# Kernel optimization log

Hardware: AMD Instinct MI355X
Metric: run time of the kernel (lower is better)

Reference implementation:

```python
import jax, jax.numpy as jnp
import numpy as np

N, D, H, O, E = 50000, 128, 256, 128, 800000


def setup_inputs() -> dict:
    key = jax.random.key(0)
    ks = jax.random.split(key, 8)
    x = jax.random.normal(ks[0], (N, D), dtype=jnp.float32)
    edge_index = jax.random.randint(ks[1], (2, E), 0, N, dtype=jnp.int64)
    s = lambda k, shp: jax.random.normal(k, shp, dtype=jnp.float32) / np.sqrt(shp[0])
    return {
        "x": x,
        "edge_index": edge_index,
        "W1_l": s(ks[2], (D, H)),
        "W1_r": s(ks[3], (D, H)),
        "b1": jnp.zeros((H,), jnp.float32),
        "W2_l": s(ks[4], (H, O)),
        "W2_r": s(ks[5], (H, O)),
        "b2": jnp.zeros((O,), jnp.float32),
    }


def _sage_conv(x, src, dst, W_l, W_r, b, n_nodes):
    # mean aggregation of source messages into destination nodes
    agg = jax.ops.segment_sum(x[src], dst, num_segments=n_nodes)  # [N, F]
    cnt = jax.ops.segment_sum(jnp.ones(src.shape[0], x.dtype), dst,
                              num_segments=n_nodes)               # [N]
    agg = agg / jnp.maximum(cnt, 1.0)[:, None]
    # lin_l(agg) + lin_r(x); lin_l carries the bias (PyG SAGEConv default)
    return agg @ W_l + b + x @ W_r


def reference(x, edge_index, W1_l, W1_r, b1, W2_l, W2_r, b2):
    src, dst = edge_index[0], edge_index[1]
    h = jax.nn.relu(_sage_conv(x, src, dst, W1_l, W1_r, b1, N))
    out = _sage_conv(h, src, dst, W2_l, W2_r, b2, N)
    return out
```

## Files before the change

kernel.cpp:

```cpp
#include <hip/hip_runtime.h>


#define CAP 64
#define NB 98
#define BSH 9
#define BCAP 9216
#define CHUNK 2048

typedef __attribute__((ext_vector_type(8))) short short8;
typedef __attribute__((ext_vector_type(8))) unsigned short ushort8;
typedef __attribute__((ext_vector_type(4))) float f32x4;

__device__ __forceinline__ unsigned short f2bf(float f) {
  unsigned u = __builtin_bit_cast(unsigned, f);
  u += 0x7fff + ((u >> 16) & 1);
  return (unsigned short)(u >> 16);
}
__device__ __forceinline__ float bf2f(unsigned v) {
  return __builtin_bit_cast(float, v << 16);
}

__global__ __launch_bounds__(256) void bucket_kernel(
    const int* __restrict__ src, const int* __restrict__ dst,
    int* __restrict__ bcursor, unsigned* __restrict__ buckets, int E) {
  __shared__ unsigned pack[CHUNK];
  __shared__ unsigned char binarr[CHUNK];
  __shared__ unsigned sorted[CHUNK];
  __shared__ unsigned char sbin[CHUNK];
  __shared__ int hist[NB];
  __shared__ int scn[NB + 1];
  __shared__ int gbase[NB];
  const int t = threadIdx.x;
  const int e0 = blockIdx.x * CHUNK;
  const int n = min(CHUNK, E - e0);

  for (int i = t; i < NB; i += 256) hist[i] = 0;
  __syncthreads();
  for (int i = t; i < n; i += 256) {
    int s = src[e0 + i];
    int d = dst[e0 + i];
    int b = d >> BSH;
    pack[i] = ((unsigned)(d & 511) << 16) | (unsigned)s;
    binarr[i] = (unsigned char)b;
    atomicAdd(&hist[b], 1);
  }
  __syncthreads();
  if (t == 0) {
    int a = 0;
    for (int b = 0; b < NB; ++b) { scn[b] = a; a += hist[b]; }
    scn[NB] = a;
  }
  __syncthreads();
  if (t < NB) { gbase[t] = atomicAdd(&bcursor[t], hist[t]); hist[t] = 0; }
  __syncthreads();
  for (int i = t; i < n; i += 256) {
    int b = binarr[i];
    int pos = scn[b] + atomicAdd(&hist[b], 1);
    sorted[pos] = pack[i];
    sbin[pos] = (unsigned char)b;
  }
  __syncthreads();
  for (int i = t; i < n; i += 256) {
    int b = sbin[i];
    int off = gbase[b] + (i - scn[b]);
    if (off < BCAP) buckets[(size_t)b * BCAP + off] = sorted[i];
  }
}

__global__ __launch_bounds__(256) void csr_kernel(
    const int* __restrict__ bcursor, const unsigned* __restrict__ buckets,
    unsigned short* __restrict__ elist, int* __restrict__ deg, int N) {
  __shared__ unsigned short csr[128 * CAP];
  __shared__ int cur[128];
  const int t = threadIdx.x;
  const int b = blockIdx.x >> 2;
  const int q = blockIdx.x & 3;
  if (t < 128) cur[t] = 0;
  __syncthreads();
  const int cnt = min(bcursor[b], BCAP);
  const unsigned* bp = buckets + (size_t)b * BCAP;
  for (int i = t; i < cnt; i += 256) {
    unsigned p = bp[i];
    int lo = p >> 16;
    if ((lo >> 7) == q) {
      int r = lo & 127;
      int pos = atomicAdd(&cur[r], 1);
      if (pos < CAP) csr[r * CAP + pos] = (unsigned short)(p & 0xffffu);
    }
  }
  __syncthreads();
  const int node0 = (b << BSH) + (q << 7);
  const int nn = min(128, N - node0);
  if (nn <= 0) return;
  if (t < nn) deg[node0 + t] = min(cur[t], CAP);
  int4* dst4 = reinterpret_cast<int4*>(elist + (size_t)node0 * CAP);
  const int4* src4 = reinterpret_cast<const int4*>(csr);
  for (int i = t; i < nn * 8; i += 256) dst4[i] = src4[i];
}

__global__ __launch_bounds__(256) void convert_x_kernel(const float* __restrict__ x,
                                                        unsigned short* __restrict__ xb,
                                                        int* __restrict__ bcursor,
                                                        int n8) {
  int i = blockIdx.x * 256 + threadIdx.x;
  if (blockIdx.x == 0 && threadIdx.x < 128) bcursor[threadIdx.x] = 0;
  if (i >= n8) return;
  const float4* p = reinterpret_cast<const float4*>(x) + (size_t)i * 2;
  float4 a = p[0], b = p[1];
  union { unsigned short u[8]; int4 v; } r;
  r.u[0]=f2bf(a.x); r.u[1]=f2bf(a.y); r.u[2]=f2bf(a.z); r.u[3]=f2bf(a.w);
  r.u[4]=f2bf(b.x); r.u[5]=f2bf(b.y); r.u[6]=f2bf(b.z); r.u[7]=f2bf(b.w);
  reinterpret_cast<int4*>(xb)[i] = r.v;
}

__global__ __launch_bounds__(256) void convert_w_kernel(
    const float* __restrict__ W1l, const float* __restrict__ W1r,
    const float* __restrict__ W2l, const float* __restrict__ W2r,
    unsigned short* __restrict__ Wt1, unsigned short* __restrict__ Wt2) {
  int idx = blockIdx.x * 256 + threadIdx.x;
  int ch = idx >> 8, k = idx & 255;
  float v1 = (k < 128) ? W1l[k * 256 + ch] : W1r[(k - 128) * 256 + ch];
  Wt1[idx] = f2bf(v1);
  float v2 = (ch < 128) ? W2l[k * 128 + ch] : W2r[k * 128 + (ch - 128)];
  Wt2[idx] = f2bf(v2);
}

template<int MODE>
__global__ __launch_bounds__(256) void aggregate_kernel(
    const unsigned short* __restrict__ feat, const int* __restrict__ deg_,
    const unsigned short* __restrict__ elist, const unsigned short* __restrict__ hr,
    const float* __restrict__ bias, void* __restrict__ outp, int N) {
  const int node = (blockIdx.x * blockDim.x + threadIdx.x) >> 6;
  const int lane = threadIdx.x & 63;
  if (node >= N) return;
  const int deg = deg_[node];
  const unsigned short* el = elist + (size_t)node * CAP;
  const unsigned* f = reinterpret_cast<const unsigned*>(feat);
  float s0x=0.f,s0y=0.f,s1x=0.f,s1y=0.f,s2x=0.f,s2y=0.f,s3x=0.f,s3y=0.f;
  int j = 0;
  for (; j + 7 < deg; j += 8) {
    ushort8 e8 = *reinterpret_cast<const ushort8*>(el + j);
    unsigned v0 = f[(size_t)e8[0] * 64 + lane];
    unsigned v1 = f[(size_t)e8[1] * 64 + lane];
    unsigned v2 = f[(size_t)e8[2] * 64 + lane];
    unsigned v3 = f[(size_t)e8[3] * 64 + lane];
    unsigned v4 = f[(size_t)e8[4] * 64 + lane];
    unsigned v5 = f[(size_t)e8[5] * 64 + lane];
    unsigned v6 = f[(size_t)e8[6] * 64 + lane];
    unsigned v7 = f[(size_t)e8[7] * 64 + lane];
    s0x += bf2f(v0 & 0xffffu); s0y += bf2f(v0 >> 16);
    s1x += bf2f(v1 & 0xffffu); s1y += bf2f(v1 >> 16);
    s2x += bf2f(v2 & 0xffffu); s2y += bf2f(v2 >> 16);
    s3x += bf2f(v3 & 0xffffu); s3y += bf2f(v3 >> 16);
    s0x += bf2f(v4 & 0xffffu); s0y += bf2f(v4 >> 16);
    s1x += bf2f(v5 & 0xffffu); s1y += bf2f(v5 >> 16);
    s2x += bf2f(v6 & 0xffffu); s2y += bf2f(v6 >> 16);
    s3x += bf2f(v7 & 0xffffu); s3y += bf2f(v7 >> 16);
  }
  for (; j < deg; ++j) {
    unsigned v0 = f[(size_t)el[j] * 64 + lane];
    s0x += bf2f(v0 & 0xffffu); s0y += bf2f(v0 >> 16);
  }
  float inv = 1.0f / (float)max(deg, 1);
  float rx = (s0x + s1x + s2x + s3x) * inv;
  float ry = (s0y + s1y + s2y + s3y) * inv;
  if constexpr (MODE == 0) {
    unsigned r = (unsigned)f2bf(rx) | ((unsigned)f2bf(ry) << 16);
    reinterpret_cast<unsigned*>(outp)[(size_t)node * 64 + lane] = r;
  } else {
    unsigned res = reinterpret_cast<const unsigned*>(hr)[(size_t)node * 64 + lane];
    float2 bb = reinterpret_cast<const float2*>(bias)[lane];
    float2 o;
    o.x = rx + bf2f(res & 0xffffu) + bb.x;
    o.y = ry + bf2f(res >> 16) + bb.y;
    reinterpret_cast<float2*>(outp)[(size_t)node * 64 + lane] = o;
  }
}

__global__ __launch_bounds__(256, 2) void fused_gemm_kernel(
    const unsigned short* __restrict__ aggb, const unsigned short* __restrict__ xb,
    const unsigned short* __restrict__ Wt1, const unsigned short* __restrict__ Wt2,
    const float* __restrict__ b1,
    unsigned short* __restrict__ hw, unsigned short* __restrict__ hr, int N) {
  __shared__ int4 As4[512];
  __shared__ int4 Bs4[2048];
  __shared__ int4 hL4[2048];
  char* As = reinterpret_cast<char*>(As4);
  char* Bs = reinterpret_cast<char*>(Bs4);
  char* hL = reinterpret_cast<char*>(hL4);
  const int t = threadIdx.x;
  const int lane = t & 63;
  const int hi = lane >> 4;
  const int lo = lane & 15;
  const int wv = t >> 6;
  const int n0 = blockIdx.x * 64;
  const int cw = wv * 64;

  f32x4 acc[4][4];
  #pragma unroll
  for (int m = 0; m < 4; ++m)
    #pragma unroll
    for (int n = 0; n < 4; ++n)
      acc[m][n] = (f32x4){0.f, 0.f, 0.f, 0.f};

  for (int k0 = 0; k0 < 256; k0 += 64) {
    const unsigned short* Asrc = (k0 < 128) ? aggb : xb;
    const int kk0 = k0 & 127;
    #pragma unroll
    for (int i = 0; i < 2; ++i) {
      int chunk = i * 256 + t;
      int r = chunk >> 3, c16 = chunk & 7;
      int row = n0 + r; if (row >= N) row = N - 1;
      int4 v = *reinterpret_cast<const int4*>(Asrc + (size_t)row * 128 + kk0 + c16 * 8);
      *reinterpret_cast<int4*>(As + r * 128 + ((c16 * 16) ^ ((r & 7) << 4))) = v;
    }
    #pragma unroll
    for (int i = 0; i < 8; ++i) {
      int chunk = i * 256 + t;
      int cc = chunk >> 3, c16 = chunk & 7;
      int4 v = *reinterpret_cast<const int4*>(Wt1 + (size_t)cc * 256 + k0 + c16 * 8);
      *reinterpret_cast<int4*>(Bs + cc * 128 + ((c16 * 16) ^ ((cc & 7) << 4))) = v;
    }
    __syncthreads();
    #pragma unroll
    for (int kk = 0; kk < 64; kk += 32) {
      const int kb = (kk + hi * 8) * 2;
      short8 af[4], bfr[4];
      #pragma unroll
      for (int m = 0; m < 4; ++m) {
        int r = m * 16 + lo;
        af[m] = *reinterpret_cast<const short8*>(As + r * 128 + (kb ^ ((r & 7) << 4)));
      }
      #pragma unroll
      for (int n = 0; n < 4; ++n) {
        int c = cw + n * 16 + lo;
        bfr[n] = *reinterpret_cast<const short8*>(Bs + c * 128 + (kb ^ ((c & 7) << 4)));
      }
      #pragma unroll
      for (int m = 0; m < 4; ++m)
        #pragma unroll
        for (int n = 0; n < 4; ++n)
          acc[m][n] = __builtin_amdgcn_mfma_f32_16x16x32_bf16(af[m], bfr[n], acc[m][n], 0, 0, 0);
    }
    __syncthreads();
  }

  #pragma unroll
  for (int n = 0; n < 4; ++n) {
    const int col = cw + n * 16 + lo;
    const float bv = b1[col];
    const int seg = col >> 6;
    const int wb = (col & 63) * 2;
    #pragma unroll
    for (int m = 0; m < 4; ++m) {
      f32x4 v = acc[m][n];
      #pragma unroll
      for (int j = 0; j < 4; ++j) {
        int row = m * 16 + hi * 4 + j;
        float f = fmaxf(v[j] + bv, 0.0f);
        *reinterpret_cast<unsigned short*>(
            hL + row * 512 + seg * 128 + (wb ^ ((row & 7) << 4))) = f2bf(f);
      }
    }
  }
  __syncthreads();

  f32x4 acc2[4][4];
  #pragma unroll
  for (int m = 0; m < 4; ++m)
    #pragma unroll
    for (int n = 0; n < 4; ++n)
      acc2[m][n] = (f32x4){0.f, 0.f, 0.f, 0.f};

  for (int k0 = 0; k0 < 256; k0 += 64) {
    #pragma unroll
    for (int i = 0; i < 8; ++i) {
      int chunk = i * 256 + t;
      int cc = chunk >> 3, c16 = chunk & 7;
      int4 v = *reinterpret_cast<const int4*>(Wt2 + (size_t)cc * 256 + k0 + c16 * 8);
      *reinterpret_cast<int4*>(Bs + cc * 128 + ((c16 * 16) ^ ((cc & 7) << 4))) = v;
    }
    __syncthreads();
    #pragma unroll
    for (int kk = 0; kk < 64; kk += 32) {
      const int kb = (kk + hi * 8) * 2;
      short8 af[4], bfr[4];
      #pragma unroll
      for (int m = 0; m < 4; ++m) {
        int r = m * 16 + lo;
        af[m] = *reinterpret_cast<const short8*>(hL + r * 512 + k0 * 2 + (kb ^ ((r & 7) << 4)));
      }
      #pragma unroll
      for (int n = 0; n < 4; ++n) {
        int c = cw + n * 16 + lo;
        bfr[n] = *reinterpret_cast<const short8*>(Bs + c * 128 + (kb ^ ((c & 7) << 4)));
      }
      #pragma unroll
      for (int m = 0; m < 4; ++m)
        #pragma unroll
        for (int n = 0; n < 4; ++n)
          acc2[m][n] = __builtin_amdgcn_mfma_f32_16x16x32_bf16(af[m], bfr[n], acc2[m][n], 0, 0, 0);
    }
    __syncthreads();
  }

  unsigned short* dstp = (cw < 128) ? hw : hr;
  const int cbase = cw & 127;
  #pragma unroll
  for (int n = 0; n < 4; ++n) {
    const int col = cbase + n * 16 + lo;
    #pragma unroll
    for (int m = 0; m < 4; ++m) {
      f32x4 v = acc2[m][n];
      #pragma unroll
      for (int j = 0; j < 4; ++j) {
        int row = n0 + m * 16 + hi * 4 + j;
        if (row < N) dstp[(size_t)row * 128 + col] = f2bf(v[j]);
      }
    }
  }
}

extern "C" void kernel_launch(void* const* d_in, const int* in_sizes, int n_in,
                              void* d_out, int out_size, void* d_ws, size_t ws_size,
                              hipStream_t stream) {
  const float* x   = (const float*)d_in[0];
  const int*   ei  = (const int*)d_in[1];
  const float* W1l = (const float*)d_in[2];
  const float* W1r = (const float*)d_in[3];
  const float* b1  = (const float*)d_in[4];
  const float* W2l = (const float*)d_in[5];
  const float* W2r = (const float*)d_in[6];
  const float* b2  = (const float*)d_in[7];
  float* out = (float*)d_out;

  const int N = in_sizes[0] / 128;
  const int E = in_sizes[1] / 2;
  const int* src = ei;
  const int* dst = ei + E;

  int* iws = (int*)d_ws;
  int* bcursor = iws;
  unsigned* buckets = (unsigned*)(iws + 128);
  int* deg = (int*)(buckets + (size_t)NB * BCAP);
  unsigned short* elist = (unsigned short*)(deg + ((N + 64) & ~63));
  unsigned short* xb   = elist + (size_t)N * CAP;
  unsigned short* aggb = xb + (size_t)N * 128;
  unsigned short* hw   = aggb + (size_t)N * 128;
  unsigned short* hr   = hw + (size_t)N * 128;
  unsigned short* Wt1  = hr + (size_t)N * 128;
  unsigned short* Wt2  = Wt1 + 65536;

  convert_x_kernel<<<(N * 128 / 8 + 255) / 256, 256, 0, stream>>>(x, xb, bcursor, N * 128 / 8);
  convert_w_kernel<<<256, 256, 0, stream>>>(W1l, W1r, W2l, W2r, Wt1, Wt2);

  bucket_kernel<<<(E + CHUNK - 1) / CHUNK, 256, 0, stream>>>(src, dst, bcursor, buckets, E);
  csr_kernel<<<NB * 4, 256, 0, stream>>>(bcursor, buckets, elist, deg, N);

  const int aggBlocks = (N * 64 + 255) / 256;
  const int MB = (N + 63) / 64;

  aggregate_kernel<0><<<aggBlocks, 256, 0, stream>>>(xb, deg, elist, nullptr, nullptr, (void*)aggb, N);
  fused_gemm_kernel<<<MB, 256, 0, stream>>>(aggb, xb, Wt1, Wt2, b1, hw, hr, N);
  aggregate_kernel<1><<<aggBlocks, 256, 0, stream>>>(hw, deg, elist, hr, b2, (void*)out, N);
}
```

Baseline: 146.6 us.

## Fuse first-layer aggregation into GEMM kernel and merge conversion kernels

The first mean-aggregation is moved into the fused GEMM kernel: each block gathers neighbor features for its 64 rows directly into a combined LDS tile holding [agg | x], which is later reused for the hidden activations. This removes the aggb intermediate write and read and one kernel launch. The x and weight conversion kernels are also merged into one prep kernel. In exchange, the gather now runs inside a GEMM kernel limited by launch bounds to 2 blocks per CU, with only 4 waves handling 16 rows each, so latency hiding for the random gathers may be worse.

```diff
diff --git a/kernel.cpp b/kernel.cpp
--- a/kernel.cpp
+++ b/kernel.cpp
@@ -18,6 +18,33 @@
 }
 __device__ __forceinline__ float bf2f(unsigned v) {
   return __builtin_bit_cast(float, v << 16);
+}
+
+__global__ __launch_bounds__(256) void prep_kernel(
+    const float* __restrict__ x, unsigned short* __restrict__ xb,
+    const float* __restrict__ W1l, const float* __restrict__ W1r,
+    const float* __restrict__ W2l, const float* __restrict__ W2r,
+    unsigned short* __restrict__ Wt1, unsigned short* __restrict__ Wt2,
+    int* __restrict__ bcursor, int n8) {
+  const int b = blockIdx.x;
+  const int t = threadIdx.x;
+  if (b == 0 && t < 128) bcursor[t] = 0;
+  if (b < 256) {
+    int idx = b * 256 + t;
+    int ch = idx >> 8, k = idx & 255;
+    Wt1[idx] = f2bf((k < 128) ? W1l[k * 256 + ch] : W1r[(k - 128) * 256 + ch]);
+    Wt2[idx] = f2bf((ch < 128) ? W2l[k * 128 + ch] : W2r[k * 128 + (ch - 128)]);
+  } else {
+    int i = (b - 256) * 256 + t;
+    if (i < n8) {
+      const float4* p = reinterpret_cast<const float4*>(x) + (size_t)i * 2;
+      float4 a = p[0], bb = p[1];
+      union { unsigned short u[8]; int4 v; } r;
+      r.u[0]=f2bf(a.x); r.u[1]=f2bf(a.y); r.u[2]=f2bf(a.z); r.u[3]=f2bf(a.w);
+      r.u[4]=f2bf(bb.x); r.u[5]=f2bf(bb.y); r.u[6]=f2bf(bb.z); r.u[7]=f2bf(bb.w);
+      reinterpret_cast<int4*>(xb)[i] = r.v;
+    }
+  }
 }
 
 __global__ __launch_bounds__(256) void bucket_kernel(
@@ -98,38 +125,10 @@
   for (int i = t; i < nn * 8; i += 256) dst4[i] = src4[i];
 }
 
-__global__ __launch_bounds__(256) void convert_x_kernel(const float* __restrict__ x,
-                                                        unsigned short* __restrict__ xb,
-                                                        int* __restrict__ bcursor,
-                                                        int n8) {
-  int i = blockIdx.x * 256 + threadIdx.x;
-  if (blockIdx.x == 0 && threadIdx.x < 128) bcursor[threadIdx.x] = 0;
-  if (i >= n8) return;
-  const float4* p = reinterpret_cast<const float4*>(x) + (size_t)i * 2;
-  float4 a = p[0], b = p[1];
-  union { unsigned short u[8]; int4 v; } r;
-  r.u[0]=f2bf(a.x); r.u[1]=f2bf(a.y); r.u[2]=f2bf(a.z); r.u[3]=f2bf(a.w);
-  r.u[4]=f2bf(b.x); r.u[5]=f2bf(b.y); r.u[6]=f2bf(b.z); r.u[7]=f2bf(b.w);
-  reinterpret_cast<int4*>(xb)[i] = r.v;
-}
-
-__global__ __launch_bounds__(256) void convert_w_kernel(
-    const float* __restrict__ W1l, const float* __restrict__ W1r,
-    const float* __restrict__ W2l, const float* __restrict__ W2r,
-    unsigned short* __restrict__ Wt1, unsigned short* __restrict__ Wt2) {
-  int idx = blockIdx.x * 256 + threadIdx.x;
-  int ch = idx >> 8, k = idx & 255;
-  float v1 = (k < 128) ? W1l[k * 256 + ch] : W1r[(k - 128) * 256 + ch];
-  Wt1[idx] = f2bf(v1);
-  float v2 = (ch < 128) ? W2l[k * 128 + ch] : W2r[k * 128 + (ch - 128)];
-  Wt2[idx] = f2bf(v2);
-}
-
-template<int MODE>
-__global__ __launch_bounds__(256) void aggregate_kernel(
+__global__ __launch_bounds__(256) void aggregate2_kernel(
     const unsigned short* __restrict__ feat, const int* __restrict__ deg_,
     const unsigned short* __restrict__ elist, const unsigned short* __restrict__ hr,
-    const float* __restrict__ bias, void* __restrict__ outp, int N) {
+    const float* __restrict__ bias, float* __restrict__ outp, int N) {
   const int node = (blockIdx.x * blockDim.x + threadIdx.x) >> 6;
   const int lane = threadIdx.x & 63;
   if (node >= N) return;
@@ -164,30 +163,24 @@
   float inv = 1.0f / (float)max(deg, 1);
   float rx = (s0x + s1x + s2x + s3x) * inv;
   float ry = (s0y + s1y + s2y + s3y) * inv;
-  if constexpr (MODE == 0) {
-    unsigned r = (unsigned)f2bf(rx) | ((unsigned)f2bf(ry) << 16);
-    reinterpret_cast<unsigned*>(outp)[(size_t)node * 64 + lane] = r;
-  } else {
-    unsigned res = reinterpret_cast<const unsigned*>(hr)[(size_t)node * 64 + lane];
-    float2 bb = reinterpret_cast<const float2*>(bias)[lane];
-    float2 o;
-    o.x = rx + bf2f(res & 0xffffu) + bb.x;
-    o.y = ry + bf2f(res >> 16) + bb.y;
-    reinterpret_cast<float2*>(outp)[(size_t)node * 64 + lane] = o;
-  }
+  unsigned res = reinterpret_cast<const unsigned*>(hr)[(size_t)node * 64 + lane];
+  float2 bb = reinterpret_cast<const float2*>(bias)[lane];
+  float2 o;
+  o.x = rx + bf2f(res & 0xffffu) + bb.x;
+  o.y = ry + bf2f(res >> 16) + bb.y;
+  reinterpret_cast<float2*>(outp)[(size_t)node * 64 + lane] = o;
 }
 
 __global__ __launch_bounds__(256, 2) void fused_gemm_kernel(
-    const unsigned short* __restrict__ aggb, const unsigned short* __restrict__ xb,
+    const unsigned short* __restrict__ xb,
     const unsigned short* __restrict__ Wt1, const unsigned short* __restrict__ Wt2,
-    const float* __restrict__ b1,
+    const float* __restrict__ b1, const int* __restrict__ deg_,
+    const unsigned short* __restrict__ elist,
     unsigned short* __restrict__ hw, unsigned short* __restrict__ hr, int N) {
-  __shared__ int4 As4[512];
+  __shared__ int4 AH4[2048];
   __shared__ int4 Bs4[2048];
-  __shared__ int4 hL4[2048];
-  char* As = reinterpret_cast<char*>(As4);
+  char* AH = reinterpret_cast<char*>(AH4);
   char* Bs = reinterpret_cast<char*>(Bs4);
-  char* hL = reinterpret_cast<char*>(hL4);
   const int t = threadIdx.x;
   const int lane = t & 63;
   const int hi = lane >> 4;
@@ -196,6 +189,56 @@
   const int n0 = blockIdx.x * 64;
   const int cw = wv * 64;
 
+  #pragma unroll
+  for (int i = 0; i < 4; ++i) {
+    int chunk = i * 256 + t;
+    int r = chunk >> 4, c16 = chunk & 15;
+    int node = n0 + r; if (node >= N) node = N - 1;
+    int4 v = *reinterpret_cast<const int4*>(xb + (size_t)node * 128 + c16 * 8);
+    *reinterpret_cast<int4*>(AH + r * 512 + 256 + (c16 >> 3) * 128 +
+                             (((c16 & 7) * 16) ^ ((r & 7) << 4))) = v;
+  }
+  {
+    const unsigned* f = reinterpret_cast<const unsigned*>(xb);
+    for (int q = 0; q < 16; ++q) {
+      const int r = wv * 16 + q;
+      int node = n0 + r; if (node >= N) node = N - 1;
+      const int dg = deg_[node];
+      const unsigned short* el = elist + (size_t)node * CAP;
+      float s0x=0.f,s0y=0.f,s1x=0.f,s1y=0.f,s2x=0.f,s2y=0.f,s3x=0.f,s3y=0.f;
+      int j = 0;
+      for (; j + 7 < dg; j += 8) {
+        ushort8 e8 = *reinterpret_cast<const ushort8*>(el + j);
+        unsigned v0 = f[(size_t)e8[0] * 64 + lane];
+        unsigned v1 = f[(size_t)e8[1] * 64 + lane];
+        unsigned v2 = f[(size_t)e8[2] * 64 + lane];
+        unsigned v3 = f[(size_t)e8[3] * 64 + lane];
+        unsigned v4 = f[(size_t)e8[4] * 64 + lane];
+        unsigned v5 = f[(size_t)e8[5] * 64 + lane];
+        unsigned v6 = f[(size_t)e8[6] * 64 + lane];
+        unsigned v7 = f[(size_t)e8[7] * 64 + lane];
+        s0x += bf2f(v0 & 0xffffu); s0y += bf2f(v0 >> 16);
+        s1x += bf2f(v1 & 0xffffu); s1y += bf2f(v1 >> 16);
+        s2x += bf2f(v2 & 0xffffu); s2y += bf2f(v2 >> 16);
+        s3x += bf2f(v3 & 0xffffu); s3y += bf2f(v3 >> 16);
+        s0x += bf2f(v4 & 0xffffu); s0y += bf2f(v4 >> 16);
+        s1x += bf2f(v5 & 0xffffu); s1y += bf2f(v5 >> 16);
+        s2x += bf2f(v6 & 0xffffu); s2y += bf2f(v6 >> 16);
+        s3x += bf2f(v7 & 0xffffu); s3y += bf2f(v7 >> 16);
+      }
+      for (; j < dg; ++j) {
+        unsigned v0 = f[(size_t)el[j] * 64 + lane];
+        s0x += bf2f(v0 & 0xffffu); s0y += bf2f(v0 >> 16);
+      }
+      float inv = 1.0f / (float)max(dg, 1);
+      float rx = (s0x + s1x + s2x + s3x) * inv;
+      float ry = (s0y + s1y + s2y + s3y) * inv;
+      unsigned rr = (unsigned)f2bf(rx) | ((unsigned)f2bf(ry) << 16);
+      *reinterpret_cast<unsigned*>(AH + r * 512 + (lane >> 5) * 128 +
+                                   ((4 * (lane & 31)) ^ ((r & 7) << 4))) = rr;
+    }
+  }
+
   f32x4 acc[4][4];
   #pragma unroll
   for (int m = 0; m < 4; ++m)
@@ -204,16 +247,6 @@
       acc[m][n] = (f32x4){0.f, 0.f, 0.f, 0.f};
 
   for (int k0 = 0; k0 < 256; k0 += 64) {
-    const unsigned short* Asrc = (k0 < 128) ? aggb : xb;
-    const int kk0 = k0 & 127;
-    #pragma unroll
-    for (int i = 0; i < 2; ++i) {
-      int chunk = i * 256 + t;
-      int r = chunk >> 3, c16 = chunk & 7;
-      int row = n0 + r; if (row >= N) row = N - 1;
-      int4 v = *reinterpret_cast<const int4*>(Asrc + (size_t)row * 128 + kk0 + c16 * 8);
-      *reinterpret_cast<int4*>(As + r * 128 + ((c16 * 16) ^ ((r & 7) << 4))) = v;
-    }
     #pragma unroll
     for (int i = 0; i < 8; ++i) {
       int chunk = i * 256 + t;
@@ -229,7 +262,7 @@
       #pragma unroll
       for (int m = 0; m < 4; ++m) {
         int r = m * 16 + lo;
-        af[m] = *reinterpret_cast<const short8*>(As + r * 128 + (kb ^ ((r & 7) << 4)));
+        af[m] = *reinterpret_cast<const short8*>(AH + r * 512 + k0 * 2 + (kb ^ ((r & 7) << 4)));
       }
       #pragma unroll
       for (int n = 0; n < 4; ++n) {
@@ -259,7 +292,7 @@
         int row = m * 16 + hi * 4 + j;
         float f = fmaxf(v[j] + bv, 0.0f);
         *reinterpret_cast<unsigned short*>(
-            hL + row * 512 + seg * 128 + (wb ^ ((row & 7) << 4))) = f2bf(f);
+            AH + row * 512 + seg * 128 + (wb ^ ((row & 7) << 4))) = f2bf(f);
       }
     }
   }
@@ -288,7 +321,7 @@
       #pragma unroll
       for (int m = 0; m < 4; ++m) {
         int r = m * 16 + lo;
-        af[m] = *reinterpret_cast<const short8*>(hL + r * 512 + k0 * 2 + (kb ^ ((r & 7) << 4)));
+        af[m] = *reinterpret_cast<const short8*>(AH + r * 512 + k0 * 2 + (kb ^ ((r & 7) << 4)));
       }
       #pragma unroll
       for (int n = 0; n < 4; ++n) {
@@ -345,22 +378,21 @@
   int* deg = (int*)(buckets + (size_t)NB * BCAP);
   unsigned short* elist = (unsigned short*)(deg + ((N + 64) & ~63));
   unsigned short* xb   = elist + (size_t)N * CAP;
-  unsigned short* aggb = xb + (size_t)N * 128;
-  unsigned short* hw   = aggb + (size_t)N * 128;
+  unsigned short* hw   = xb + (size_t)N * 128;
   unsigned short* hr   = hw + (size_t)N * 128;
   unsigned short* Wt1  = hr + (size_t)N * 128;
   unsigned short* Wt2  = Wt1 + 65536;
 
-  convert_x_kernel<<<(N * 128 / 8 + 255) / 256, 256, 0, stream>>>(x, xb, bcursor, N * 128 / 8);
-  convert_w_kernel<<<256, 256, 0, stream>>>(W1l, W1r, W2l, W2r, Wt1, Wt2);
+  const int n8 = N * 128 / 8;
+  prep_kernel<<<256 + (n8 + 255) / 256, 256, 0, stream>>>(
+      x, xb, W1l, W1r, W2l, W2r, Wt1, Wt2, bcursor, n8);
 
   bucket_kernel<<<(E + CHUNK - 1) / CHUNK, 256, 0, stream>>>(src, dst, bcursor, buckets, E);
   csr_kernel<<<NB * 4, 256, 0, stream>>>(bcursor, buckets, elist, deg, N);
 
+  const int MB = (N + 63) / 64;
+  fused_gemm_kernel<<<MB, 256, 0, stream>>>(xb, Wt1, Wt2, b1, deg, elist, hw, hr, N);
+
   const int aggBlocks = (N * 64 + 255) / 256;
-  const int MB = (N + 63) / 64;
-
-  aggregate_kernel<0><<<aggBlocks, 256, 0, stream>>>(xb, deg, elist, nullptr, nullptr, (void*)aggb, N);
-  fused_gemm_kernel<<<MB, 256, 0, stream>>>(aggb, xb, Wt1, Wt2, b1, hw, hr, N);
-  aggregate_kernel<1><<<aggBlocks, 256, 0, stream>>>(hw, deg, elist, hr, b2, (void*)out, N);
-}
+  aggregate2_kernel<<<aggBlocks, 256, 0, stream>>>(hw, deg, elist, hr, b2, out, N);
+}
```

Result: slower. 212.3 us (+44.8%).

## Pad edge lists to a dummy zero row and software-pipeline the gather loop

Applied to the files above, without the earlier changes.

The CSR builder now pads each node's edge list up to a multiple of 8 (minimum 8) with index N, which points to a new zeroed dummy row appended to the bf16 feature buffers. The aggregate kernel loads the whole 64-entry edge list at once, then alternates two register sets of gathers and accumulates, so the loads for the next group of 8 are in flight while the current group is summed. This removes the scalar tail loop and overlaps gather latency with arithmetic, at the cost of extra dummy-row loads and more registers. The x and weight conversion kernels are also merged into one launch that zeroes the dummy rows.

```diff
diff --git a/kernel.cpp b/kernel.cpp
--- a/kernel.cpp
+++ b/kernel.cpp
@@ -18,6 +18,39 @@
 }
 __device__ __forceinline__ float bf2f(unsigned v) {
   return __builtin_bit_cast(float, v << 16);
+}
+
+__global__ __launch_bounds__(256) void prep_kernel(
+    const float* __restrict__ x, unsigned short* __restrict__ xb,
+    const float* __restrict__ W1l, const float* __restrict__ W1r,
+    const float* __restrict__ W2l, const float* __restrict__ W2r,
+    unsigned short* __restrict__ Wt1, unsigned short* __restrict__ Wt2,
+    int* __restrict__ bcursor, unsigned short* __restrict__ hw, int n8, int N) {
+  const int b = blockIdx.x;
+  const int t = threadIdx.x;
+  if (b == 0) {
+    if (t < 128) bcursor[t] = 0;
+    if (t < 64) {
+      reinterpret_cast<unsigned*>(xb + (size_t)N * 128)[t] = 0u;
+      reinterpret_cast<unsigned*>(hw + (size_t)N * 128)[t] = 0u;
+    }
+  }
+  if (b < 256) {
+    int idx = b * 256 + t;
+    int ch = idx >> 8, k = idx & 255;
+    Wt1[idx] = f2bf((k < 128) ? W1l[k * 256 + ch] : W1r[(k - 128) * 256 + ch]);
+    Wt2[idx] = f2bf((ch < 128) ? W2l[k * 128 + ch] : W2r[k * 128 + (ch - 128)]);
+  } else {
+    int i = (b - 256) * 256 + t;
+    if (i < n8) {
+      const float4* p = reinterpret_cast<const float4*>(x) + (size_t)i * 2;
+      float4 a = p[0], bb = p[1];
+      union { unsigned short u[8]; int4 v; } r;
+      r.u[0]=f2bf(a.x); r.u[1]=f2bf(a.y); r.u[2]=f2bf(a.z); r.u[3]=f2bf(a.w);
+      r.u[4]=f2bf(bb.x); r.u[5]=f2bf(bb.y); r.u[6]=f2bf(bb.z); r.u[7]=f2bf(bb.w);
+      reinterpret_cast<int4*>(xb)[i] = r.v;
+    }
+  }
 }
 
 __global__ __launch_bounds__(256) void bucket_kernel(
@@ -89,6 +122,14 @@
     }
   }
   __syncthreads();
+  if (t < 128) {
+    int d = min(cur[t], CAP);
+    int dgc = (d + 7) & ~7;
+    if (dgc < 8) dgc = 8;
+    if (dgc > CAP) dgc = CAP;
+    for (int p = d; p < dgc; ++p) csr[t * CAP + p] = (unsigned short)N;
+  }
+  __syncthreads();
   const int node0 = (b << BSH) + (q << 7);
   const int nn = min(128, N - node0);
   if (nn <= 0) return;
@@ -98,32 +139,20 @@
   for (int i = t; i < nn * 8; i += 256) dst4[i] = src4[i];
 }
 
-__global__ __launch_bounds__(256) void convert_x_kernel(const float* __restrict__ x,
-                                                        unsigned short* __restrict__ xb,
-                                                        int* __restrict__ bcursor,
-                                                        int n8) {
-  int i = blockIdx.x * 256 + threadIdx.x;
-  if (blockIdx.x == 0 && threadIdx.x < 128) bcursor[threadIdx.x] = 0;
-  if (i >= n8) return;
-  const float4* p = reinterpret_cast<const float4*>(x) + (size_t)i * 2;
-  float4 a = p[0], b = p[1];
-  union { unsigned short u[8]; int4 v; } r;
-  r.u[0]=f2bf(a.x); r.u[1]=f2bf(a.y); r.u[2]=f2bf(a.z); r.u[3]=f2bf(a.w);
-  r.u[4]=f2bf(b.x); r.u[5]=f2bf(b.y); r.u[6]=f2bf(b.z); r.u[7]=f2bf(b.w);
-  reinterpret_cast<int4*>(xb)[i] = r.v;
-}
-
-__global__ __launch_bounds__(256) void convert_w_kernel(
-    const float* __restrict__ W1l, const float* __restrict__ W1r,
-    const float* __restrict__ W2l, const float* __restrict__ W2r,
-    unsigned short* __restrict__ Wt1, unsigned short* __restrict__ Wt2) {
-  int idx = blockIdx.x * 256 + threadIdx.x;
-  int ch = idx >> 8, k = idx & 255;
-  float v1 = (k < 128) ? W1l[k * 256 + ch] : W1r[(k - 128) * 256 + ch];
-  Wt1[idx] = f2bf(v1);
-  float v2 = (ch < 128) ? W2l[k * 128 + ch] : W2r[k * 128 + (ch - 128)];
-  Wt2[idx] = f2bf(v2);
-}
+#define GLD(P, EV) \
+  P##0 = f[(size_t)(EV)[0] * 64 + lane]; P##1 = f[(size_t)(EV)[1] * 64 + lane]; \
+  P##2 = f[(size_t)(EV)[2] * 64 + lane]; P##3 = f[(size_t)(EV)[3] * 64 + lane]; \
+  P##4 = f[(size_t)(EV)[4] * 64 + lane]; P##5 = f[(size_t)(EV)[5] * 64 + lane]; \
+  P##6 = f[(size_t)(EV)[6] * 64 + lane]; P##7 = f[(size_t)(EV)[7] * 64 + lane];
+#define ACC(P) \
+  s0x += bf2f(P##0 & 0xffffu); s0y += bf2f(P##0 >> 16); \
+  s1x += bf2f(P##1 & 0xffffu); s1y += bf2f(P##1 >> 16); \
+  s2x += bf2f(P##2 & 0xffffu); s2y += bf2f(P##2 >> 16); \
+  s3x += bf2f(P##3 & 0xffffu); s3y += bf2f(P##3 >> 16); \
+  s0x += bf2f(P##4 & 0xffffu); s0y += bf2f(P##4 >> 16); \
+  s1x += bf2f(P##5 & 0xffffu); s1y += bf2f(P##5 >> 16); \
+  s2x += bf2f(P##6 & 0xffffu); s2y += bf2f(P##6 >> 16); \
+  s3x += bf2f(P##7 & 0xffffu); s3y += bf2f(P##7 >> 16);
 
 template<int MODE>
 __global__ __launch_bounds__(256) void aggregate_kernel(
@@ -134,33 +163,33 @@
   const int lane = threadIdx.x & 63;
   if (node >= N) return;
   const int deg = deg_[node];
-  const unsigned short* el = elist + (size_t)node * CAP;
+  int dgc = (deg + 7) & ~7; if (dgc < 8) dgc = 8;
   const unsigned* f = reinterpret_cast<const unsigned*>(feat);
+  const int4* el4 = reinterpret_cast<const int4*>(elist + (size_t)node * CAP);
+  int4 p0 = el4[0], p1 = el4[1], p2 = el4[2], p3 = el4[3],
+       p4 = el4[4], p5 = el4[5], p6 = el4[6], p7 = el4[7];
+  ushort8 c0 = __builtin_bit_cast(ushort8, p0), c1 = __builtin_bit_cast(ushort8, p1),
+          c2 = __builtin_bit_cast(ushort8, p2), c3 = __builtin_bit_cast(ushort8, p3),
+          c4 = __builtin_bit_cast(ushort8, p4), c5 = __builtin_bit_cast(ushort8, p5),
+          c6 = __builtin_bit_cast(ushort8, p6), c7 = __builtin_bit_cast(ushort8, p7);
   float s0x=0.f,s0y=0.f,s1x=0.f,s1y=0.f,s2x=0.f,s2y=0.f,s3x=0.f,s3y=0.f;
-  int j = 0;
-  for (; j + 7 < deg; j += 8) {
-    ushort8 e8 = *reinterpret_cast<const ushort8*>(el + j);
-    unsigned v0 = f[(size_t)e8[0] * 64 + lane];
-    unsigned v1 = f[(size_t)e8[1] * 64 + lane];
-    unsigned v2 = f[(size_t)e8[2] * 64 + lane];
-    unsigned v3 = f[(size_t)e8[3] * 64 + lane];
-    unsigned v4 = f[(size_t)e8[4] * 64 + lane];
-    unsigned v5 = f[(size_t)e8[5] * 64 + lane];
-    unsigned v6 = f[(size_t)e8[6] * 64 + lane];
-    unsigned v7 = f[(size_t)e8[7] * 64 + lane];
-    s0x += bf2f(v0 & 0xffffu); s0y += bf2f(v0 >> 16);
-    s1x += bf2f(v1 & 0xffffu); s1y += bf2f(v1 >> 16);
-    s2x += bf2f(v2 & 0xffffu); s2y += bf2f(v2 >> 16);
-    s3x += bf2f(v3 & 0xffffu); s3y += bf2f(v3 >> 16);
-    s0x += bf2f(v4 & 0xffffu); s0y += bf2f(v4 >> 16);
-    s1x += bf2f(v5 & 0xffffu); s1y += bf2f(v5 >> 16);
-    s2x += bf2f(v6 & 0xffffu); s2y += bf2f(v6 >> 16);
-    s3x += bf2f(v7 & 0xffffu); s3y += bf2f(v7 >> 16);
-  }
-  for (; j < deg; ++j) {
-    unsigned v0 = f[(size_t)el[j] * 64 + lane];
-    s0x += bf2f(v0 & 0xffffu); s0y += bf2f(v0 >> 16);
-  }
+  unsigned a0,a1,a2,a3,a4,a5,a6,a7, b0,b1,b2,b3,b4,b5,b6,b7;
+  GLD(a, c0);
+  if (dgc > 8)  { GLD(b, c1); }
+  ACC(a);
+  if (dgc > 16) { GLD(a, c2); }
+  if (dgc > 8)  { ACC(b); }
+  if (dgc > 24) { GLD(b, c3); }
+  if (dgc > 16) { ACC(a); }
+  if (dgc > 32) { GLD(a, c4); }
+  if (dgc > 24) { ACC(b); }
+  if (dgc > 40) { GLD(b, c5); }
+  if (dgc > 32) { ACC(a); }
+  if (dgc > 48) { GLD(a, c6); }
+  if (dgc > 40) { ACC(b); }
+  if (dgc > 56) { GLD(b, c7); }
+  if (dgc > 48) { ACC(a); }
+  if (dgc > 56) { ACC(b); }
   float inv = 1.0f / (float)max(deg, 1);
   float rx = (s0x + s1x + s2x + s3x) * inv;
   float ry = (s0y + s1y + s2y + s3y) * inv;
@@ -345,14 +374,15 @@
   int* deg = (int*)(buckets + (size_t)NB * BCAP);
   unsigned short* elist = (unsigned short*)(deg + ((N + 64) & ~63));
   unsigned short* xb   = elist + (size_t)N * CAP;
-  unsigned short* aggb = xb + (size_t)N * 128;
+  unsigned short* aggb = xb + (size_t)(N + 8) * 128;
   unsigned short* hw   = aggb + (size_t)N * 128;
-  unsigned short* hr   = hw + (size_t)N * 128;
+  unsigned short* hr   = hw + (size_t)(N + 8) * 128;
   unsigned short* Wt1  = hr + (size_t)N * 128;
   unsigned short* Wt2  = Wt1 + 65536;
 
-  convert_x_kernel<<<(N * 128 / 8 + 255) / 256, 256, 0, stream>>>(x, xb, bcursor, N * 128 / 8);
-  convert_w_kernel<<<256, 256, 0, stream>>>(W1l, W1r, W2l, W2r, Wt1, Wt2);
+  const int n8 = N * 128 / 8;
+  prep_kernel<<<256 + (n8 + 255) / 256, 256, 0, stream>>>(
+      x, xb, W1l, W1r, W2l, W2r, Wt1, Wt2, bcursor, hw, n8, N);
 
   bucket_kernel<<<(E + CHUNK - 1) / CHUNK, 256, 0, stream>>>(src, dst, bcursor, buckets, E);
   csr_kernel<<<NB * 4, 256, 0, stream>>>(bcursor, buckets, elist, deg, N);
```

Result: faster. 127.9 us (-12.7%).
